# Kernel optimization log

Hardware: AMD Instinct MI355X
Metric: run time of the kernel (lower is better)

The kernel has to match this reference:

```python
import jax, jax.numpy as jnp
import numpy as np

EPS = 1e-06
GEO_TEMP = 0.1
TOP_K = 32
ATTN_DIM = 256
CHANNELS = 1024
LN_EPS = 1e-05  # torch LayerNorm default


def _layernorm(x, g, b):
    mu = jnp.mean(x, axis=-1, keepdims=True)
    var = jnp.mean(jnp.square(x - mu), axis=-1, keepdims=True)
    return (x - mu) * jax.lax.rsqrt(var + LN_EPS) * g + b


def _flatten_rays(plucker):
    # plucker: [B,6,h,w] -> moments [B,N,3], dirs [B,N,3]
    b, _, h, w = plucker.shape
    rays = jnp.transpose(plucker, (0, 2, 3, 1)).reshape(b, h * w, 6)
    d = rays[..., :3]
    n = jnp.linalg.norm(d, axis=-1, keepdims=True)
    dirs = d / jnp.maximum(n, EPS)  # F.normalize semantics
    return rays[..., 3:], dirs


def _epipolar_bias(plucker_query, plucker_key):
    m_q, d_q = _flatten_rays(plucker_query)
    m_k, d_k = _flatten_rays(plucker_key)
    # reciprocal[b,i,j] = |d_q_i . m_k_j + d_k_j . m_q_i|
    reciprocal = jnp.abs(jnp.einsum('bic,bjc->bij', d_q, m_k) +
                         jnp.einsum('bjc,bic->bij', d_k, m_q))
    nq = jnp.linalg.norm(m_q, axis=-1)[:, :, None]  # [B,N,1]
    nk = jnp.linalg.norm(m_k, axis=-1)[:, None, :]  # [B,1,N]
    reciprocal = reciprocal / (nq + nk + EPS)
    geo_bias = -reciprocal / GEO_TEMP
    B, N, _ = geo_bias.shape
    if 0 < TOP_K < N:
        # keep the TOP_K smallest reciprocal entries per query row
        _, keep = jax.lax.top_k(-reciprocal, TOP_K)  # [B,N,K]
        b_idx = jnp.arange(B)[:, None, None]
        n_idx = jnp.arange(N)[None, :, None]
        drop = jnp.ones((B, N, N), dtype=bool).at[b_idx, n_idx, keep].set(False)
        geo_bias = jnp.where(drop, jnp.float32(-10000.0), geo_bias)
    return geo_bias


def setup_inputs() -> dict:
    key = jax.random.key(0)
    ks = jax.random.split(key, 12)
    B, C, h, w = 4, CHANNELS, 48, 48
    D = ATTN_DIM
    inp = {
        'query_map': jax.random.normal(ks[0], (B, C, h, w), jnp.float32),
        'key_value_map': jax.random.normal(ks[1], (B, C, h, w), jnp.float32),
        'plucker_query': jax.random.normal(ks[2], (B, 6, h, w), jnp.float32),
        'plucker_key': jax.random.normal(ks[3], (B, 6, h, w), jnp.float32),
        'ln_q_g': jnp.ones((C,), jnp.float32), 'ln_q_b': jnp.zeros((C,), jnp.float32),
        'ln_k_g': jnp.ones((C,), jnp.float32), 'ln_k_b': jnp.zeros((C,), jnp.float32),
        'Wq': jax.random.normal(ks[4], (D, C), jnp.float32) * (C ** -0.5),
        'bq': jnp.zeros((D,), jnp.float32),
        'Wk': jax.random.normal(ks[5], (D, C), jnp.float32) * (C ** -0.5),
        'bk': jnp.zeros((D,), jnp.float32),
        'Wv': jax.random.normal(ks[6], (D, C), jnp.float32) * (C ** -0.5),
        'bv': jnp.zeros((D,), jnp.float32),
        # NOTE: module zero-inits out_proj; randomized here for a non-trivial baseline
        'Wo': jax.random.normal(ks[7], (C, D), jnp.float32) * (D ** -0.5),
        'bo': jnp.zeros((C,), jnp.float32),
    }
    return inp


def reference(query_map, key_value_map, plucker_query, plucker_key,
              ln_q_g, ln_q_b, ln_k_g, ln_k_b,
              Wq, bq, Wk, bk, Wv, bv, Wo, bo):
    b, c, h, w = query_map.shape
    scale = ATTN_DIM ** (-0.5)
    # [B,C,H,W] -> [B,N,C]
    q_tokens = jnp.transpose(query_map.reshape(b, c, h * w), (0, 2, 1))
    kv_tokens = jnp.transpose(key_value_map.reshape(b, c, h * w), (0, 2, 1))
    q = _layernorm(q_tokens, ln_q_g, ln_q_b) @ Wq.T + bq
    k = _layernorm(kv_tokens, ln_k_g, ln_k_b) @ Wk.T + bk
    v = kv_tokens @ Wv.T + bv
    logits = jnp.einsum('bid,bjd->bij', q, k) * scale
    logits = logits + _epipolar_bias(plucker_query, plucker_key)
    attn = jax.nn.softmax(logits, axis=-1)
    fused = jnp.einsum('bij,bjd->bid', attn, v) @ Wo.T + bo  # [B,N,C]
    return jnp.transpose(fused, (0, 2, 1)).reshape(b, c, h, w)
```

## Files before the change

kernel.cpp:

```cpp
#include <hip/hip_runtime.h>

typedef unsigned short u16;
typedef unsigned int u32;
typedef unsigned long long u64;
typedef _Float16 f16;
typedef __attribute__((ext_vector_type(8))) _Float16 half8;
typedef __attribute__((ext_vector_type(4))) float f32x4;

#define HW 2304
#define CC 1024
#define DD 256
#define NB 4
#define CANDCAP 256
#define RANKC 33
#define GATE 0.099f

__device__ __forceinline__ float mul_s(float a, float b) {
  float r; asm volatile("v_mul_f32 %0, %1, %2" : "=v"(r) : "v"(a), "v"(b)); return r;
}
__device__ __forceinline__ float add_s(float a, float b) {
  float r; asm volatile("v_add_f32 %0, %1, %2" : "=v"(r) : "v"(a), "v"(b)); return r;
}
__device__ __forceinline__ void split16(float a, u16& hi, u16& lo) {
  f16 h = (f16)a;
  float hf = (float)h;
  f16 l = (f16)(a - hf);
  __builtin_memcpy(&hi, &h, 2);
  __builtin_memcpy(&lo, &l, 2);
}

__global__ void prep_weights(const float* __restrict__ wq, const float* __restrict__ wk,
                             const float* __restrict__ wv, const float* __restrict__ wo,
                             u16* __restrict__ qh, u16* __restrict__ ql,
                             u16* __restrict__ kh, u16* __restrict__ kl,
                             u16* __restrict__ vh, u16* __restrict__ vl,
                             u16* __restrict__ oh, u16* __restrict__ ol) {
  int idx = blockIdx.x * 256 + threadIdx.x;
  for (int i = idx; i < 4 * 262144; i += 262144) {
    int which = i >> 18, loc = i & 262143;
    const float* s = (which == 0) ? wq : (which == 1) ? wk : (which == 2) ? wv : wo;
    u16* dh = (which == 0) ? qh : (which == 1) ? kh : (which == 2) ? vh : oh;
    u16* dl = (which == 0) ? ql : (which == 1) ? kl : (which == 2) ? vl : ol;
    u16 h, l; split16(s[loc], h, l);
    dh[loc] = h; dl[loc] = l;
  }
}

__global__ void prep_rays(const float* __restrict__ pq, const float* __restrict__ pk,
                          float* __restrict__ qray, float* __restrict__ kray) {
#pragma clang fp contract(off)
  int t = blockIdx.x * 256 + threadIdx.x;
  const float* src = blockIdx.y ? pk : pq;
  float* dst = blockIdx.y ? kray : qray;
  int b = t / HW, i = t % HW;
  const float* sp = src + (size_t)b * 6 * HW + i;
  float d0 = sp[0], d1 = sp[HW], d2 = sp[2 * HW];
  float m0 = sp[3 * HW], m1 = sp[4 * HW], m2 = sp[5 * HW];
  float nd = __fsqrt_rn(add_s(add_s(mul_s(d0, d0), mul_s(d1, d1)), mul_s(d2, d2)));
  float nc = fmaxf(nd, 1e-6f);
  float ix = d0 / nc, iy = d1 / nc, iz = d2 / nc;
  float nm = __fsqrt_rn(add_s(add_s(mul_s(m0, m0), mul_s(m1, m1)), mul_s(m2, m2)));
  float4* dp = (float4*)(dst + (size_t)t * 12);
  dp[0] = make_float4(m0, m1, m2, nm);
  dp[1] = make_float4(ix, iy, iz, 0.f);
  dp[2] = make_float4(d0, d1, d2, 0.f);
}

__global__ __launch_bounds__(256) void ln_stats(const float* __restrict__ qmap,
                                                const float* __restrict__ kvmap,
                                                float* __restrict__ mu_q, float* __restrict__ rs_q,
                                                float* __restrict__ mu_k, float* __restrict__ rs_k) {
  const float* src = blockIdx.z ? kvmap : qmap;
  float* mu = blockIdx.z ? mu_k : mu_q;
  float* rs = blockIdx.z ? rs_k : rs_q;
  int b = blockIdx.y;
  int i0 = blockIdx.x * 32;
  int lane = threadIdx.x & 31, strip = threadIdx.x >> 5;
  const float* p = src + (size_t)b * CC * HW + i0 + lane;
  float s = 0.f, s2 = 0.f;
  for (int c = strip; c < CC; c += 8) {
    float v = p[(size_t)c * HW];
    s += v; s2 += v * v;
  }
  __shared__ float rsum[8][32], rsq[8][32];
  rsum[strip][lane] = s; rsq[strip][lane] = s2;
  __syncthreads();
  if (threadIdx.x < 32) {
    float ts = 0.f, tq = 0.f;
    for (int k = 0; k < 8; ++k) { ts += rsum[k][lane]; tq += rsq[k][lane]; }
    float m = ts * (1.f / 1024.f);
    float var = fmaxf(tq * (1.f / 1024.f) - m * m, 0.f);
    mu[b * HW + i0 + lane] = m;
    rs[b * HW + i0 + lane] = rsqrtf(var + 1e-5f);
  }
}

__global__ __launch_bounds__(256) void proj_mfma(
    const float* __restrict__ qmap, const float* __restrict__ kvmap,
    const float* __restrict__ gq, const float* __restrict__ bgq,
    const float* __restrict__ gk, const float* __restrict__ bgk,
    const u16* __restrict__ wqh, const u16* __restrict__ wql,
    const u16* __restrict__ wkh, const u16* __restrict__ wkl,
    const u16* __restrict__ wvh, const u16* __restrict__ wvl,
    const float* __restrict__ bq, const float* __restrict__ bk, const float* __restrict__ bv,
    const float* __restrict__ muq, const float* __restrict__ rsq,
    const float* __restrict__ muk, const float* __restrict__ rsk,
    float* __restrict__ qf, float* __restrict__ kf, float* __restrict__ vf) {
  int mtile = blockIdx.x, proj = blockIdx.y, b = blockIdx.z;
  int i0 = mtile * 64;
  const float* A; const u16* Wh; const u16* Wl;
  const float* gamma; const float* beta; const float* mup; const float* rsp; const float* bias;
  float* outp;
  if (proj == 0)      { A = qmap;  Wh = wqh; Wl = wql; gamma = gq; beta = bgq; mup = muq; rsp = rsq; bias = bq; outp = qf; }
  else if (proj == 1) { A = kvmap; Wh = wkh; Wl = wkl; gamma = gk; beta = bgk; mup = muk; rsp = rsk; bias = bk; outp = kf; }
  else                { A = kvmap; Wh = wvh; Wl = wvl; gamma = nullptr; beta = nullptr; mup = nullptr; rsp = nullptr; bias = bv; outp = vf; }
  __shared__ u16 Ah[64 * 72], Al[64 * 72];
  __shared__ u16 Bh[256 * 72], Bl[256 * 72];
  __shared__ float mul[64], rsl[64];
  int tid = threadIdx.x;
  int lane = tid & 63, wid = tid >> 6;
  if (proj < 2 && tid < 64) {
    mul[tid] = mup[b * HW + i0 + tid];
    rsl[tid] = rsp[b * HW + i0 + tid];
  }
  __syncthreads();
  f32x4 acc[4][4] = {};
  int c_loc = tid >> 2;
  int i4 = (tid & 3) * 4;
  int rowA = lane & 15, kch = (lane >> 4) * 8;
  for (int ks = 0; ks < 16; ++ks) {
    int c0 = ks * 64;
    float gma = 1.f, bet = 0.f;
    if (proj < 2) { gma = gamma[c0 + c_loc]; bet = beta[c0 + c_loc]; }
    const float* ap = A + ((size_t)(b * CC + c0 + c_loc)) * HW + i0;
#pragma unroll
    for (int p = 0; p < 4; ++p) {
      int ib = p * 16 + i4;
      float4 v = *(const float4*)(ap + ib);
      float e0 = v.x, e1 = v.y, e2 = v.z, e3 = v.w;
      if (proj < 2) {
        e0 = (e0 - mul[ib + 0]) * rsl[ib + 0] * gma + bet;
        e1 = (e1 - mul[ib + 1]) * rsl[ib + 1] * gma + bet;
        e2 = (e2 - mul[ib + 2]) * rsl[ib + 2] * gma + bet;
        e3 = (e3 - mul[ib + 3]) * rsl[ib + 3] * gma + bet;
      }
      u16 h, l;
      split16(e0, h, l); Ah[(ib + 0) * 72 + c_loc] = h; Al[(ib + 0) * 72 + c_loc] = l;
      split16(e1, h, l); Ah[(ib + 1) * 72 + c_loc] = h; Al[(ib + 1) * 72 + c_loc] = l;
      split16(e2, h, l); Ah[(ib + 2) * 72 + c_loc] = h; Al[(ib + 2) * 72 + c_loc] = l;
      split16(e3, h, l); Ah[(ib + 3) * 72 + c_loc] = h; Al[(ib + 3) * 72 + c_loc] = l;
    }
#pragma unroll
    for (int p = 0; p < 8; ++p) {
      int d = p * 32 + (tid >> 3);
      int cc2 = (tid & 7) * 8;
      *(uint4*)&Bh[d * 72 + cc2] = *(const uint4*)&Wh[(size_t)d * CC + c0 + cc2];
      *(uint4*)&Bl[d * 72 + cc2] = *(const uint4*)&Wl[(size_t)d * CC + c0 + cc2];
    }
    __syncthreads();
#pragma unroll
    for (int kk = 0; kk < 2; ++kk) {
      int ko = kk * 32 + kch;
      half8 ah[4], al[4], bh[4], bl[4];
#pragma unroll
      for (int mf = 0; mf < 4; ++mf) {
        ah[mf] = *(const half8*)&Ah[(mf * 16 + rowA) * 72 + ko];
        al[mf] = *(const half8*)&Al[(mf * 16 + rowA) * 72 + ko];
      }
#pragma unroll
      for (int nf = 0; nf < 4; ++nf) {
        bh[nf] = *(const half8*)&Bh[(wid * 64 + nf * 16 + rowA) * 72 + ko];
        bl[nf] = *(const half8*)&Bl[(wid * 64 + nf * 16 + rowA) * 72 + ko];
      }
#pragma unroll
      for (int mf = 0; mf < 4; ++mf)
#pragma unroll
        for (int nf = 0; nf < 4; ++nf) {
          acc[mf][nf] = __builtin_amdgcn_mfma_f32_16x16x32_f16(ah[mf], bh[nf], acc[mf][nf], 0, 0, 0);
          acc[mf][nf] = __builtin_amdgcn_mfma_f32_16x16x32_f16(ah[mf], bl[nf], acc[mf][nf], 0, 0, 0);
          acc[mf][nf] = __builtin_amdgcn_mfma_f32_16x16x32_f16(al[mf], bh[nf], acc[mf][nf], 0, 0, 0);
        }
    }
    __syncthreads();
  }
  int r4 = (lane >> 4) * 4, cold = lane & 15;
#pragma unroll
  for (int nf = 0; nf < 4; ++nf) {
    int dcol = wid * 64 + nf * 16 + cold;
    float bsv = bias[dcol];
#pragma unroll
    for (int mf = 0; mf < 4; ++mf) {
#pragma unroll
      for (int r = 0; r < 4; ++r) {
        int irow = i0 + mf * 16 + r4 + r;
        outp[(size_t)(b * HW + irow) * DD + dcol] = acc[mf][nf][r] + bsv;
      }
    }
  }
}

__global__ __launch_bounds__(64) void attn_f32(
    const float* __restrict__ qf, const float* __restrict__ kf, const float* __restrict__ vf,
    const float* __restrict__ qray, const float* __restrict__ kray,
    float* __restrict__ fusedf, float* __restrict__ dfused, int* __restrict__ flags) {
#pragma clang fp contract(off)
  int i = blockIdx.x, b = blockIdx.y;
  int lane = threadIdx.x;
  __shared__ u32 hist[1024];
  __shared__ float qs[DD];
  __shared__ int kidx[RANKC];
  __shared__ float kr[RANKC];
  __shared__ float lgt[RANKC];
  __shared__ float wgt[RANKC];
  __shared__ float dw[RANKC];
  __shared__ int cidx[CANDCAP];
  __shared__ float cr[CANDCAP];
  __shared__ int s_alt, s_last, s_hedge;
  int tok = b * HW + i;
  ((float4*)qs)[lane] = ((const float4*)(qf + (size_t)tok * DD))[lane];
  const float* qp = qray + (size_t)tok * 12;
  float4 mq = ((const float4*)qp)[0];
  float4 dq = ((const float4*)qp)[1];
#pragma unroll
  for (int k = 0; k < 16; ++k) hist[lane * 16 + k] = 0;
  __syncthreads();
  const float* krb = kray + (size_t)b * HW * 12;
  auto rcomp = [&](int j) -> float {
    const float4* kp4 = (const float4*)(krb + (size_t)j * 12);
    float4 km = kp4[0], kd = kp4[1];
    float p0 = mul_s(dq.x, km.x), p1 = mul_s(dq.y, km.y), p2 = mul_s(dq.z, km.z);
    float s1 = add_s(add_s(p0, p2), p1);
    float q0 = mul_s(kd.x, mq.x), q1 = mul_s(kd.y, mq.y), q2 = mul_s(kd.z, mq.z);
    float s2 = add_s(add_s(q0, q2), q1);
    float num = fabsf(add_s(s1, s2));
    float den = add_s(add_s(mq.w, km.w), 1e-6f);
    return num / den;
  };
  for (int t = 0; t < 36; ++t) {
    float r = rcomp(t * 64 + lane);
    atomicAdd(&hist[__float_as_uint(r) >> 22], 1u);
  }
  __syncthreads();
  int own = 0;
#pragma unroll
  for (int k = 0; k < 16; ++k) own += (int)hist[lane * 16 + k];
  int incl = own;
  for (int off = 1; off < 64; off <<= 1) {
    int nn = __shfl_up(incl, off);
    if (lane >= off) incl += nn;
  }
  u64 bal = __ballot(incl >= RANKC);
  int srcl = __ffsll((long long)bal) - 1;
  int exclv = __shfl(incl - own, srcl);
  int bstar = -1, below = 0, cum = exclv;
  for (int k = 0; k < 16; ++k) {
    int cnt = (int)hist[srcl * 16 + k];
    if (bstar < 0 && cum + cnt >= RANKC) { bstar = srcl * 16 + k; below = cum; }
    cum += cnt;
  }
  int kc = 0, ccn = 0;
  for (int t = 0; t < 36; ++t) {
    int j = t * 64 + lane;
    float r = rcomp(j);
    int bin = (int)(__float_as_uint(r) >> 22);
    bool isk = bin < bstar, isc = bin == bstar;
    u64 bkm = __ballot(isk);
    u64 bcm = __ballot(isc);
    u64 mymask = (1ull << lane) - 1ull;
    if (isk) { int p = kc + __popcll(bkm & mymask); kidx[p] = j; kr[p] = r; }
    if (isc) { int p = ccn + __popcll(bcm & mymask); if (p < CANDCAP) { cidx[p] = j; cr[p] = r; } }
    kc += (int)__popcll(bkm);
    ccn += (int)__popcll(bcm);
  }
  __syncthreads();
  int m = RANKC - below;
  bool usec = (ccn <= CANDCAP);
  for (int s = 0; s < m; ++s) {
    float bvv = 3.402823466e38f; int bj = 0x7fffffff; int bp = -1;
    if (usec) {
      for (int p = lane; p < ccn; p += 64) {
        float v = cr[p]; int j = cidx[p];
        if (v < bvv || (v == bvv && j < bj)) { bvv = v; bj = j; bp = p; }
      }
    } else {
      for (int t = 0; t < 36; ++t) {
        int j = t * 64 + lane;
        float v = rcomp(j);
        if ((int)(__float_as_uint(v) >> 22) != bstar) continue;
        bool used = false;
        for (int u = 0; u < s; ++u) if (kidx[below + u] == j) { used = true; break; }
        if (!used && (v < bvv || (v == bvv && j < bj))) { bvv = v; bj = j; bp = -1; }
      }
    }
#pragma unroll
    for (int off = 32; off; off >>= 1) {
      float ov = __shfl_xor(bvv, off); int oj = __shfl_xor(bj, off); int op = __shfl_xor(bp, off);
      if (ov < bvv || (ov == bvv && oj < bj)) { bvv = ov; bj = oj; bp = op; }
    }
    if (lane == 0) {
      kidx[below + s] = bj; kr[below + s] = bvv;
      if (bp >= 0) cr[bp] = 3.402823466e38f;
    }
    __syncthreads();
  }
  if (lane == 0) {
    int ia = -1, ib = -1;
    for (int t = 0; t < RANKC; ++t) {
      bool gA = (ia < 0) || (kr[t] > kr[ia]) || (kr[t] == kr[ia] && kidx[t] > kidx[ia]);
      if (gA) { ib = ia; ia = t; }
      else {
        bool gB = (ib < 0) || (kr[t] > kr[ib]) || (kr[t] == kr[ib] && kidx[t] > kidx[ib]);
        if (gB) ib = t;
      }
    }
    float tau = 0.f;
    for (int u = 0; u < 2; ++u) {
      int t = u ? ib : ia;
      const float* kp = krb + (size_t)kidx[t] * 12;
      float sp = fabsf(dq.x * kp[0]) + fabsf(dq.y * kp[1]) + fabsf(dq.z * kp[2])
               + fabsf(kp[4] * mq.x) + fabsf(kp[5] * mq.y) + fabsf(kp[6] * mq.z);
      float den = (mq.w + kp[3]) + 1e-6f;
      tau += 20.0f * 5.9604645e-08f * sp / den + 4e-7f * kr[t];
    }
    s_alt = ia; s_last = ib;
    s_hedge = ((kr[ia] - kr[ib]) < tau) ? 1 : 0;
  }
  __syncthreads();
  if (lane < RANKC) {
    const float* kp = kf + (size_t)(b * HW + kidx[lane]) * DD;
    float dot = 0.f;
#pragma unroll 8
    for (int d2 = 0; d2 < DD / 4; ++d2) {
      float4 k4 = ((const float4*)kp)[d2];
      float4 q4 = ((const float4*)qs)[d2];
      dot = fmaf(k4.x, q4.x, dot);
      dot = fmaf(k4.y, q4.y, dot);
      dot = fmaf(k4.z, q4.z, dot);
      dot = fmaf(k4.w, q4.w, dot);
    }
    lgt[lane] = dot * 0.0625f - kr[lane] / 0.1f;
  }
  __syncthreads();
  if (lane == 0) {
    int ia = s_alt, ib = s_last;
    float m1 = -3.402823466e38f;
    for (int t = 0; t < RANKC; ++t) if (t != ia) m1 = fmaxf(m1, lgt[t]);
    float z1 = 0.f;
    for (int t = 0; t < RANKC; ++t) {
      float e = (t == ia) ? 0.f : expf(lgt[t] - m1);
      wgt[t] = e; z1 += e;
    }
    float iz1 = 1.f / z1;
    for (int t = 0; t < RANKC; ++t) wgt[t] *= iz1;
    if (s_hedge) {
      float m2 = -3.402823466e38f;
      for (int t = 0; t < RANKC; ++t) if (t != ib) m2 = fmaxf(m2, lgt[t]);
      float z2 = 0.f;
      for (int t = 0; t < RANKC; ++t) {
        float e = (t == ib) ? 0.f : expf(lgt[t] - m2);
        dw[t] = e; z2 += e;
      }
      float iz2 = 1.f / z2;
      for (int t = 0; t < RANKC; ++t) dw[t] = wgt[t] - dw[t] * iz2;
    }
  }
  __syncthreads();
  float4 o = make_float4(0.f, 0.f, 0.f, 0.f);
  float4 od = make_float4(0.f, 0.f, 0.f, 0.f);
  const float* vb = vf + (size_t)b * HW * DD;
  int hedge = s_hedge;
  for (int tt = 0; tt < RANKC; ++tt) {
    float wv = wgt[tt]; int j = kidx[tt];
    float4 vv = *(const float4*)(vb + (size_t)j * DD + lane * 4);
    o.x = fmaf(wv, vv.x, o.x);
    o.y = fmaf(wv, vv.y, o.y);
    o.z = fmaf(wv, vv.z, o.z);
    o.w = fmaf(wv, vv.w, o.w);
    if (hedge) {
      float dv = dw[tt];
      od.x = fmaf(dv, vv.x, od.x);
      od.y = fmaf(dv, vv.y, od.y);
      od.z = fmaf(dv, vv.z, od.z);
      od.w = fmaf(dv, vv.w, od.w);
    }
  }
  *(float4*)(fusedf + (size_t)tok * DD + lane * 4) = o;
  if (hedge) *(float4*)(dfused + (size_t)tok * DD + lane * 4) = od;
  if (lane == 0) flags[tok] = hedge;
}

__global__ __launch_bounds__(256) void hedge_gate(
    const float* __restrict__ Wo, const int* __restrict__ flags,
    const float* __restrict__ dfused, float* __restrict__ fusedf) {
  int tok = blockIdx.x;
  if (!flags[tok]) return;
  __shared__ float dfl[DD];
  __shared__ float wmax[8];
  int tid = threadIdx.x;
  dfl[tid] = dfused[(size_t)tok * DD + tid];
  __syncthreads();
  float lmax = 0.f;
  for (int k = 0; k < 4; ++k) {
    int c = k * 256 + tid;
    const float* wr = Wo + (size_t)c * DD;
    float dot = 0.f;
#pragma unroll 8
    for (int d = 0; d < DD; d += 4) {
      float4 w4 = *(const float4*)(wr + d);
      float4 f4 = *(const float4*)(dfl + d);
      dot = fmaf(w4.x, f4.x, dot);
      dot = fmaf(w4.y, f4.y, dot);
      dot = fmaf(w4.z, f4.z, dot);
      dot = fmaf(w4.w, f4.w, dot);
    }
    lmax = fmaxf(lmax, fabsf(dot));
  }
#pragma unroll
  for (int off = 32; off; off >>= 1) lmax = fmaxf(lmax, __shfl_xor(lmax, off));
  if ((tid & 63) == 0) wmax[tid >> 6] = lmax;
  __syncthreads();
  if (tid == 0) wmax[4] = fmaxf(fmaxf(wmax[0], wmax[1]), fmaxf(wmax[2], wmax[3]));
  __syncthreads();
  if (wmax[4] <= GATE) {
    fusedf[(size_t)tok * DD + tid] -= 0.5f * dfl[tid];
  }
}

__global__ __launch_bounds__(256) void out_mfma(
    const u16* __restrict__ woh, const u16* __restrict__ wol,
    const float* __restrict__ fusedf, const float* __restrict__ bo,
    float* __restrict__ out) {
  int itile = blockIdx.x, ctile = blockIdx.y, b = blockIdx.z;
  int i0 = itile * 128, c0 = ctile * 128;
  __shared__ u16 Ah[128 * 72], Al[128 * 72];
  __shared__ u16 Bh[128 * 72], Bl[128 * 72];
  int tid = threadIdx.x, lane = tid & 63, wid = tid >> 6;
  int wm = (wid >> 1) * 64, wn = (wid & 1) * 64;
  f32x4 acc[4][4] = {};
  int rowA = lane & 15, kch = (lane >> 4) * 8;
  for (int ks = 0; ks < 4; ++ks) {
    int d0 = ks * 64;
#pragma unroll
    for (int p = 0; p < 4; ++p) {
      int rr = p * 32 + (tid >> 3);
      int dc = (tid & 7) * 8;
      *(uint4*)&Ah[rr * 72 + dc] = *(const uint4*)&woh[(size_t)(c0 + rr) * DD + d0 + dc];
      *(uint4*)&Al[rr * 72 + dc] = *(const uint4*)&wol[(size_t)(c0 + rr) * DD + d0 + dc];
      const float* fp = &fusedf[(size_t)(b * HW + i0 + rr) * DD + d0 + dc];
      float4 f0 = *(const float4*)fp;
      float4 f1 = *(const float4*)(fp + 4);
      u16 h, l;
      split16(f0.x, h, l); Bh[rr * 72 + dc + 0] = h; Bl[rr * 72 + dc + 0] = l;
      split16(f0.y, h, l); Bh[rr * 72 + dc + 1] = h; Bl[rr * 72 + dc + 1] = l;
      split16(f0.z, h, l); Bh[rr * 72 + dc + 2] = h; Bl[rr * 72 + dc + 2] = l;
      split16(f0.w, h, l); Bh[rr * 72 + dc + 3] = h; Bl[rr * 72 + dc + 3] = l;
      split16(f1.x, h, l); Bh[rr * 72 + dc + 4] = h; Bl[rr * 72 + dc + 4] = l;
      split16(f1.y, h, l); Bh[rr * 72 + dc + 5] = h; Bl[rr * 72 + dc + 5] = l;
      split16(f1.z, h, l); Bh[rr * 72 + dc + 6] = h; Bl[rr * 72 + dc + 6] = l;
      split16(f1.w, h, l); Bh[rr * 72 + dc + 7] = h; Bl[rr * 72 + dc + 7] = l;
    }
    __syncthreads();
#pragma unroll
    for (int kk = 0; kk < 2; ++kk) {
      int ko = kk * 32 + kch;
      half8 ah[4], al[4], bh[4], bl[4];
#pragma unroll
      for (int mf = 0; mf < 4; ++mf) {
        ah[mf] = *(const half8*)&Ah[(wm + mf * 16 + rowA) * 72 + ko];
        al[mf] = *(const half8*)&Al[(wm + mf * 16 + rowA) * 72 + ko];
      }
#pragma unroll
      for (int nf = 0; nf < 4; ++nf) {
        bh[nf] = *(const half8*)&Bh[(wn + nf * 16 + rowA) * 72 + ko];
        bl[nf] = *(const half8*)&Bl[(wn + nf * 16 + rowA) * 72 + ko];
      }
#pragma unroll
      for (int mf = 0; mf < 4; ++mf)
#pragma unroll
        for (int nf = 0; nf < 4; ++nf) {
          acc[mf][nf] = __builtin_amdgcn_mfma_f32_16x16x32_f16(ah[mf], bh[nf], acc[mf][nf], 0, 0, 0);
          acc[mf][nf] = __builtin_amdgcn_mfma_f32_16x16x32_f16(ah[mf], bl[nf], acc[mf][nf], 0, 0, 0);
          acc[mf][nf] = __builtin_amdgcn_mfma_f32_16x16x32_f16(al[mf], bh[nf], acc[mf][nf], 0, 0, 0);
        }
    }
    __syncthreads();
  }
  int r4 = (lane >> 4) * 4, cold = lane & 15;
#pragma unroll
  for (int mf = 0; mf < 4; ++mf) {
#pragma unroll
    for (int r = 0; r < 4; ++r) {
      int crow = c0 + wm + mf * 16 + r4 + r;
      float bsv = bo[crow];
#pragma unroll
      for (int nf = 0; nf < 4; ++nf) {
        int icol = i0 + wn + nf * 16 + cold;
        out[(size_t)(b * CC + crow) * HW + icol] = acc[mf][nf][r] + bsv;
      }
    }
  }
}

extern "C" void kernel_launch(void* const* d_in, const int* in_sizes, int n_in,
                              void* d_out, int out_size, void* d_ws, size_t ws_size,
                              hipStream_t stream) {
  (void)in_sizes; (void)n_in; (void)out_size; (void)ws_size;
  const float* qmap = (const float*)d_in[0];
  const float* kvmap = (const float*)d_in[1];
  const float* pq = (const float*)d_in[2];
  const float* pk = (const float*)d_in[3];
  const float* lnqg = (const float*)d_in[4];
  const float* lnqb = (const float*)d_in[5];
  const float* lnkg = (const float*)d_in[6];
  const float* lnkb = (const float*)d_in[7];
  const float* Wq = (const float*)d_in[8];
  const float* bq = (const float*)d_in[9];
  const float* Wk = (const float*)d_in[10];
  const float* bk = (const float*)d_in[11];
  const float* Wv = (const float*)d_in[12];
  const float* bv = (const float*)d_in[13];
  const float* Wo = (const float*)d_in[14];
  const float* bo = (const float*)d_in[15];
  float* out = (float*)d_out;
  char* w = (char*)d_ws;
  size_t off = 0;
  auto take = [&](size_t n) { char* p = w + off; off += (n + 511) & ~(size_t)511; return p; };
  u16* wq_h = (u16*)take((size_t)DD * CC * 2);
  u16* wq_l = (u16*)take((size_t)DD * CC * 2);
  u16* wk_h = (u16*)take((size_t)DD * CC * 2);
  u16* wk_l = (u16*)take((size_t)DD * CC * 2);
  u16* wv_h = (u16*)take((size_t)DD * CC * 2);
  u16* wv_l = (u16*)take((size_t)DD * CC * 2);
  u16* wo_h = (u16*)take((size_t)CC * DD * 2);
  u16* wo_l = (u16*)take((size_t)CC * DD * 2);
  float* qray = (float*)take((size_t)NB * HW * 12 * 4);
  float* kray = (float*)take((size_t)NB * HW * 12 * 4);
  float* mu_q = (float*)take((size_t)NB * HW * 4);
  float* rs_q = (float*)take((size_t)NB * HW * 4);
  float* mu_k = (float*)take((size_t)NB * HW * 4);
  float* rs_k = (float*)take((size_t)NB * HW * 4);
  float* qf = (float*)take((size_t)NB * HW * DD * 4);
  float* kf = (float*)take((size_t)NB * HW * DD * 4);
  float* vf = (float*)take((size_t)NB * HW * DD * 4);
  float* fusedf = (float*)take((size_t)NB * HW * DD * 4);
  float* dfused = (float*)take((size_t)NB * HW * DD * 4);
  int* flags = (int*)take((size_t)NB * HW * 4);

  prep_weights<<<dim3(1024), 256, 0, stream>>>(Wq, Wk, Wv, Wo, wq_h, wq_l, wk_h, wk_l,
                                               wv_h, wv_l, wo_h, wo_l);
  prep_rays<<<dim3(36, 2), 256, 0, stream>>>(pq, pk, qray, kray);
  ln_stats<<<dim3(72, NB, 2), 256, 0, stream>>>(qmap, kvmap, mu_q, rs_q, mu_k, rs_k);
  proj_mfma<<<dim3(36, 3, NB), 256, 0, stream>>>(qmap, kvmap, lnqg, lnqb, lnkg, lnkb,
                                                 wq_h, wq_l, wk_h, wk_l, wv_h, wv_l,
                                                 bq, bk, bv, mu_q, rs_q, mu_k, rs_k,
                                                 qf, kf, vf);
  attn_f32<<<dim3(HW, NB), 64, 0, stream>>>(qf, kf, vf, qray, kray, fusedf, dfused, flags);
  hedge_gate<<<dim3(NB * HW), 256, 0, stream>>>(Wo, flags, dfused, fusedf);
  out_mfma<<<dim3(18, 8, NB), 256, 0, stream>>>(wo_h, wo_l, fusedf, bo, out);
}
```

Baseline: 381.2 us.

## Pack four query rows per block and replace serial lane-0 reductions with wave shuffles

Each 256-thread block now handles four query tokens, one per wavefront, each with its own shared-memory slice. All __syncthreads barriers are removed and wave-level execution is relied on instead. The lane-0 serial loops for finding the two largest kept entries and computing both softmaxes are replaced by xor-shuffle reductions. The candidate buffer is halved to keep LDS use per block manageable. The risk is that dropping barriers leaves LDS write-then-read ordering within a wave implicit, and a smaller CANDCAP sends more rows down the slow rescan fallback.

```diff
diff --git a/kernel.cpp b/kernel.cpp
--- a/kernel.cpp
+++ b/kernel.cpp
@@ -11,7 +11,7 @@
 #define CC 1024
 #define DD 256
 #define NB 4
-#define CANDCAP 256
+#define CANDCAP 128
 #define RANKC 33
 #define GATE 0.099f
 
@@ -199,31 +199,28 @@
   }
 }
 
-__global__ __launch_bounds__(64) void attn_f32(
+__global__ __launch_bounds__(256) void attn_f32(
     const float* __restrict__ qf, const float* __restrict__ kf, const float* __restrict__ vf,
     const float* __restrict__ qray, const float* __restrict__ kray,
     float* __restrict__ fusedf, float* __restrict__ dfused, int* __restrict__ flags) {
 #pragma clang fp contract(off)
-  int i = blockIdx.x, b = blockIdx.y;
-  int lane = threadIdx.x;
-  __shared__ u32 hist[1024];
-  __shared__ float qs[DD];
-  __shared__ int kidx[RANKC];
-  __shared__ float kr[RANKC];
-  __shared__ float lgt[RANKC];
-  __shared__ float wgt[RANKC];
-  __shared__ float dw[RANKC];
-  __shared__ int cidx[CANDCAP];
-  __shared__ float cr[CANDCAP];
-  __shared__ int s_alt, s_last, s_hedge;
+  int w = threadIdx.x >> 6, lane = threadIdx.x & 63;
+  int i = blockIdx.x * 4 + w, b = blockIdx.y;
+  __shared__ u32 hist[4][1024];
+  __shared__ float qs[4][DD];
+  __shared__ int kidx[4][RANKC];
+  __shared__ float kr[4][RANKC];
+  __shared__ float wgt[4][RANKC];
+  __shared__ float dws[4][RANKC];
+  __shared__ int cidx[4][CANDCAP];
+  __shared__ float cr[4][CANDCAP];
   int tok = b * HW + i;
-  ((float4*)qs)[lane] = ((const float4*)(qf + (size_t)tok * DD))[lane];
+  ((float4*)qs[w])[lane] = ((const float4*)(qf + (size_t)tok * DD))[lane];
   const float* qp = qray + (size_t)tok * 12;
   float4 mq = ((const float4*)qp)[0];
   float4 dq = ((const float4*)qp)[1];
 #pragma unroll
-  for (int k = 0; k < 16; ++k) hist[lane * 16 + k] = 0;
-  __syncthreads();
+  for (int k = 0; k < 16; ++k) hist[w][lane * 16 + k] = 0;
   const float* krb = kray + (size_t)b * HW * 12;
   auto rcomp = [&](int j) -> float {
     const float4* kp4 = (const float4*)(krb + (size_t)j * 12);
@@ -238,12 +235,11 @@
   };
   for (int t = 0; t < 36; ++t) {
     float r = rcomp(t * 64 + lane);
-    atomicAdd(&hist[__float_as_uint(r) >> 22], 1u);
-  }
-  __syncthreads();
+    atomicAdd(&hist[w][__float_as_uint(r) >> 22], 1u);
+  }
   int own = 0;
 #pragma unroll
-  for (int k = 0; k < 16; ++k) own += (int)hist[lane * 16 + k];
+  for (int k = 0; k < 16; ++k) own += (int)hist[w][lane * 16 + k];
   int incl = own;
   for (int off = 1; off < 64; off <<= 1) {
     int nn = __shfl_up(incl, off);
@@ -254,7 +250,7 @@
   int exclv = __shfl(incl - own, srcl);
   int bstar = -1, below = 0, cum = exclv;
   for (int k = 0; k < 16; ++k) {
-    int cnt = (int)hist[srcl * 16 + k];
+    int cnt = (int)hist[w][srcl * 16 + k];
     if (bstar < 0 && cum + cnt >= RANKC) { bstar = srcl * 16 + k; below = cum; }
     cum += cnt;
   }
@@ -267,19 +263,18 @@
     u64 bkm = __ballot(isk);
     u64 bcm = __ballot(isc);
     u64 mymask = (1ull << lane) - 1ull;
-    if (isk) { int p = kc + __popcll(bkm & mymask); kidx[p] = j; kr[p] = r; }
-    if (isc) { int p = ccn + __popcll(bcm & mymask); if (p < CANDCAP) { cidx[p] = j; cr[p] = r; } }
+    if (isk) { int p = kc + __popcll(bkm & mymask); kidx[w][p] = j; kr[w][p] = r; }
+    if (isc) { int p = ccn + __popcll(bcm & mymask); if (p < CANDCAP) { cidx[w][p] = j; cr[w][p] = r; } }
     kc += (int)__popcll(bkm);
     ccn += (int)__popcll(bcm);
   }
-  __syncthreads();
   int m = RANKC - below;
   bool usec = (ccn <= CANDCAP);
   for (int s = 0; s < m; ++s) {
     float bvv = 3.402823466e38f; int bj = 0x7fffffff; int bp = -1;
     if (usec) {
       for (int p = lane; p < ccn; p += 64) {
-        float v = cr[p]; int j = cidx[p];
+        float v = cr[w][p]; int j = cidx[w][p];
         if (v < bvv || (v == bvv && j < bj)) { bvv = v; bj = j; bp = p; }
       }
     } else {
@@ -288,7 +283,7 @@
         float v = rcomp(j);
         if ((int)(__float_as_uint(v) >> 22) != bstar) continue;
         bool used = false;
-        for (int u = 0; u < s; ++u) if (kidx[below + u] == j) { used = true; break; }
+        for (int u = 0; u < s; ++u) if (kidx[w][below + u] == j) { used = true; break; }
         if (!used && (v < bvv || (v == bvv && j < bj))) { bvv = v; bj = j; bp = -1; }
       }
     }
@@ -298,86 +293,90 @@
       if (ov < bvv || (ov == bvv && oj < bj)) { bvv = ov; bj = oj; bp = op; }
     }
     if (lane == 0) {
-      kidx[below + s] = bj; kr[below + s] = bvv;
-      if (bp >= 0) cr[bp] = 3.402823466e38f;
-    }
-    __syncthreads();
-  }
-  if (lane == 0) {
-    int ia = -1, ib = -1;
-    for (int t = 0; t < RANKC; ++t) {
-      bool gA = (ia < 0) || (kr[t] > kr[ia]) || (kr[t] == kr[ia] && kidx[t] > kidx[ia]);
-      if (gA) { ib = ia; ia = t; }
-      else {
-        bool gB = (ib < 0) || (kr[t] > kr[ib]) || (kr[t] == kr[ib] && kidx[t] > kidx[ib]);
-        if (gB) ib = t;
-      }
-    }
-    float tau = 0.f;
+      kidx[w][below + s] = bj; kr[w][below + s] = bvv;
+      if (bp >= 0) cr[w][bp] = 3.402823466e38f;
+    }
+  }
+  float sv = (lane < RANKC) ? kr[w][lane] : -3.402823466e38f;
+  int sj = (lane < RANKC) ? kidx[w][lane] : -1;
+  float v1 = sv; int j1 = sj; int t1 = lane;
+#pragma unroll
+  for (int off = 32; off; off >>= 1) {
+    float ov = __shfl_xor(v1, off); int oj = __shfl_xor(j1, off); int ot = __shfl_xor(t1, off);
+    if (ov > v1 || (ov == v1 && oj > j1)) { v1 = ov; j1 = oj; t1 = ot; }
+  }
+  int ia = t1;
+  float v2 = (lane < RANKC && lane != ia) ? kr[w][lane] : -3.402823466e38f;
+  int j2 = (lane < RANKC && lane != ia) ? kidx[w][lane] : -1;
+  int t2 = lane;
+#pragma unroll
+  for (int off = 32; off; off >>= 1) {
+    float ov = __shfl_xor(v2, off); int oj = __shfl_xor(j2, off); int ot = __shfl_xor(t2, off);
+    if (ov > v2 || (ov == v2 && oj > j2)) { v2 = ov; j2 = oj; t2 = ot; }
+  }
+  int ib = t2;
+  float tau = 0.f;
+  {
+    int tt2[2] = { ia, ib };
+#pragma unroll
     for (int u = 0; u < 2; ++u) {
-      int t = u ? ib : ia;
-      const float* kp = krb + (size_t)kidx[t] * 12;
+      const float* kp = krb + (size_t)kidx[w][tt2[u]] * 12;
       float sp = fabsf(dq.x * kp[0]) + fabsf(dq.y * kp[1]) + fabsf(dq.z * kp[2])
                + fabsf(kp[4] * mq.x) + fabsf(kp[5] * mq.y) + fabsf(kp[6] * mq.z);
       float den = (mq.w + kp[3]) + 1e-6f;
-      tau += 20.0f * 5.9604645e-08f * sp / den + 4e-7f * kr[t];
-    }
-    s_alt = ia; s_last = ib;
-    s_hedge = ((kr[ia] - kr[ib]) < tau) ? 1 : 0;
-  }
-  __syncthreads();
+      tau += 20.0f * 5.9604645e-08f * sp / den + 4e-7f * kr[w][tt2[u]];
+    }
+  }
+  int hedge = ((kr[w][ia] - kr[w][ib]) < tau) ? 1 : 0;
+  float lgt_l = -3.402823466e38f;
   if (lane < RANKC) {
-    const float* kp = kf + (size_t)(b * HW + kidx[lane]) * DD;
+    const float* kp = kf + (size_t)(b * HW + kidx[w][lane]) * DD;
+    const float* qsp = qs[w];
     float dot = 0.f;
 #pragma unroll 8
     for (int d2 = 0; d2 < DD / 4; ++d2) {
       float4 k4 = ((const float4*)kp)[d2];
-      float4 q4 = ((const float4*)qs)[d2];
+      float4 q4 = ((const float4*)qsp)[d2];
       dot = fmaf(k4.x, q4.x, dot);
       dot = fmaf(k4.y, q4.y, dot);
       dot = fmaf(k4.z, q4.z, dot);
       dot = fmaf(k4.w, q4.w, dot);
     }
-    lgt[lane] = dot * 0.0625f - kr[lane] / 0.1f;
-  }
-  __syncthreads();
-  if (lane == 0) {
-    int ia = s_alt, ib = s_last;
-    float m1 = -3.402823466e38f;
-    for (int t = 0; t < RANKC; ++t) if (t != ia) m1 = fmaxf(m1, lgt[t]);
-    float z1 = 0.f;
-    for (int t = 0; t < RANKC; ++t) {
-      float e = (t == ia) ? 0.f : expf(lgt[t] - m1);
-      wgt[t] = e; z1 += e;
-    }
-    float iz1 = 1.f / z1;
-    for (int t = 0; t < RANKC; ++t) wgt[t] *= iz1;
-    if (s_hedge) {
-      float m2 = -3.402823466e38f;
-      for (int t = 0; t < RANKC; ++t) if (t != ib) m2 = fmaxf(m2, lgt[t]);
-      float z2 = 0.f;
-      for (int t = 0; t < RANKC; ++t) {
-        float e = (t == ib) ? 0.f : expf(lgt[t] - m2);
-        dw[t] = e; z2 += e;
-      }
-      float iz2 = 1.f / z2;
-      for (int t = 0; t < RANKC; ++t) dw[t] = wgt[t] - dw[t] * iz2;
-    }
-  }
-  __syncthreads();
+    lgt_l = dot * 0.0625f - kr[w][lane] / 0.1f;
+  }
+  {
+    float mv = (lane < RANKC && lane != ia) ? lgt_l : -3.402823466e38f;
+#pragma unroll
+    for (int off = 32; off; off >>= 1) mv = fmaxf(mv, __shfl_xor(mv, off));
+    float e1 = (lane < RANKC && lane != ia) ? expf(lgt_l - mv) : 0.f;
+    float z1 = e1;
+#pragma unroll
+    for (int off = 32; off; off >>= 1) z1 += __shfl_xor(z1, off);
+    float w1 = e1 / z1;
+    if (lane < RANKC) wgt[w][lane] = w1;
+    if (hedge) {
+      float mv2 = (lane < RANKC && lane != ib) ? lgt_l : -3.402823466e38f;
+#pragma unroll
+      for (int off = 32; off; off >>= 1) mv2 = fmaxf(mv2, __shfl_xor(mv2, off));
+      float e2 = (lane < RANKC && lane != ib) ? expf(lgt_l - mv2) : 0.f;
+      float z2 = e2;
+#pragma unroll
+      for (int off = 32; off; off >>= 1) z2 += __shfl_xor(z2, off);
+      if (lane < RANKC) dws[w][lane] = w1 - e2 / z2;
+    }
+  }
   float4 o = make_float4(0.f, 0.f, 0.f, 0.f);
   float4 od = make_float4(0.f, 0.f, 0.f, 0.f);
   const float* vb = vf + (size_t)b * HW * DD;
-  int hedge = s_hedge;
   for (int tt = 0; tt < RANKC; ++tt) {
-    float wv = wgt[tt]; int j = kidx[tt];
+    float wv = wgt[w][tt]; int j = kidx[w][tt];
     float4 vv = *(const float4*)(vb + (size_t)j * DD + lane * 4);
     o.x = fmaf(wv, vv.x, o.x);
     o.y = fmaf(wv, vv.y, o.y);
     o.z = fmaf(wv, vv.z, o.z);
     o.w = fmaf(wv, vv.w, o.w);
     if (hedge) {
-      float dv = dw[tt];
+      float dv = dws[w][tt];
       od.x = fmaf(dv, vv.x, od.x);
       od.y = fmaf(dv, vv.y, od.y);
       od.z = fmaf(dv, vv.z, od.z);
@@ -554,7 +553,7 @@
                                                  wq_h, wq_l, wk_h, wk_l, wv_h, wv_l,
                                                  bq, bk, bv, mu_q, rs_q, mu_k, rs_k,
                                                  qf, kf, vf);
-  attn_f32<<<dim3(HW, NB), 64, 0, stream>>>(qf, kf, vf, qray, kray, fusedf, dfused, flags);
+  attn_f32<<<dim3(HW / 4, NB), 256, 0, stream>>>(qf, kf, vf, qray, kray, fusedf, dfused, flags);
   hedge_gate<<<dim3(NB * HW), 256, 0, stream>>>(Wo, flags, dfused, fusedf);
   out_mfma<<<dim3(18, 8, NB), 256, 0, stream>>>(wo_h, wo_l, fusedf, bo, out);
 }
```

Result: slower. 431.3 us (+13.1%).
